# Performance work log

Measured on AMD Instinct MI355X. Metric: run time of the kernel, lower is better.

The kernel has to match this reference:

```python
import jax, jax.numpy as jnp
import numpy as np

MARGIN = 0.8  # TripletMarginMiner(margin=0.8, type_of_triplets='semihard')
Z_DIM = 512
N_CONCEPT = 64
NUM_TASK, NUM_SHOT, NUM_WAY = 16, 5, 5


def _triplet_indices(num_shot, num_way):
    # labels = torch.arange(num_way).repeat(num_shot) -> tile pattern
    labels = np.tile(np.arange(num_way), num_shot)
    N = labels.shape[0]
    same = labels[:, None] == labels[None, :]
    pos = same & ~np.eye(N, dtype=bool)          # a != p, same label
    neg = ~same                                  # different label
    a, p, n = np.nonzero(pos[:, :, None] & neg[:, None, :])  # all candidate triplets
    return jnp.asarray(a), jnp.asarray(p), jnp.asarray(n)


def setup_inputs() -> dict:
    key = jax.random.key(0)
    ks = jax.random.split(key, 12)
    d = Z_DIM
    s = lambda fan: 1.0 / np.sqrt(fan)
    inp = {
        'input_data': jax.random.normal(ks[0], (NUM_TASK, NUM_SHOT, NUM_WAY, d), jnp.float32),
        # proj_inner: Linear(3d -> 2d), ReLU, Linear(2d -> d)
        'W1': jax.random.normal(ks[1], (3 * d, 2 * d), jnp.float32) * s(3 * d),
        'b1': jnp.zeros((2 * d,), jnp.float32),
        'W2': jax.random.normal(ks[2], (2 * d, d), jnp.float32) * s(2 * d),
        'b2': jnp.zeros((d,), jnp.float32),
        # proj_outer: Linear(d -> 2d), ReLU, Linear(2d -> d)
        'W3': jax.random.normal(ks[3], (d, 2 * d), jnp.float32) * s(d),
        'b3': jnp.zeros((2 * d,), jnp.float32),
        'W4': jax.random.normal(ks[4], (2 * d, d), jnp.float32) * s(2 * d),
        'b4': jnp.zeros((d,), jnp.float32),
        # cls: Linear(d -> n_concept)
        'Wc': jax.random.normal(ks[5], (d, N_CONCEPT), jnp.float32) * s(d),
        'bc': jnp.zeros((N_CONCEPT,), jnp.float32),
    }
    return inp


def reference(input_data, W1, b1, W2, b2, W3, b3, W4, b4, Wc, bc):
    num_task, num_shot, num_way, d = input_data.shape
    x = input_data.reshape(num_task, num_shot * num_way, d)  # [K, N, d]
    a, p, n = _triplet_indices(num_shot, num_way)            # fixed triplet set [T]

    # --- semihard mining (no grad; binary mask so no grad path anyway) ---
    # LpDistance default: normalize embeddings, then L2 distance
    xn = x / jnp.linalg.norm(x, axis=-1, keepdims=True)
    sq = jnp.sum(xn * xn, axis=-1)                           # [K, N]
    D2 = sq[:, :, None] + sq[:, None, :] - 2.0 * jnp.einsum('kid,kjd->kij', xn, xn)
    D = jnp.sqrt(jnp.clip(D2, 0.0))                          # [K, N, N]
    tm = D[:, a, n] - D[:, a, p]                             # an_dist - ap_dist, [K, T]
    mask = ((tm > 0.0) & (tm <= MARGIN)).astype(x.dtype)     # semihard: 0 < margin <= 0.8

    # --- gather triplet embeddings (unnormalized), concat [x_a, x_p, x_n] ---
    feat = jnp.concatenate([x[:, a], x[:, p], x[:, n]], axis=-1)  # [K, T, 3d]

    # proj_inner then masked sum over mined triplets per task
    h = jax.nn.relu(feat @ W1 + b1) @ W2 + b2                # [K, T, d]
    pooled = jnp.einsum('ktd,kt->kd', h, mask)               # [K, d]

    o = jax.nn.relu(pooled @ W3 + b3) @ W4 + b4              # [K, d]
    score = o @ Wc + bc                                      # [K, n_concept]
    return jax.nn.softmax(score, axis=-1)
```

## Files before the change

### kernel.cpp

```cpp
#include <hip/hip_runtime.h>
#include <math.h>

#define NT 16
#define NR 25
#define DZ 512
#define D2Z 1024
#define NC 64

typedef short bf16x8 __attribute__((ext_vector_type(8)));
typedef float f32x4  __attribute__((ext_vector_type(4)));

#define TP  76
#define XSP 520
#define XP2 136
#define CP  68

static __device__ inline unsigned short f2bf(float v) {
    union { float f; unsigned u; } x; x.f = v;
    unsigned r = x.u + 0x7fffu + ((x.u >> 16) & 1u);
    return (unsigned short)(r >> 16);
}
static __device__ inline float bf2f(unsigned short h) {
    union { float f; unsigned u; } x; x.u = ((unsigned)h) << 16; return x.f;
}

__global__ __launch_bounds__(256) void k_prep(
    const float* __restrict__ x, const float* __restrict__ W1,
    unsigned short* __restrict__ W1h, unsigned short* __restrict__ W1l,
    float* __restrict__ Dm)
{
    __shared__ unsigned short th[64 * TP], tl[64 * TP];
    int vb = blockIdx.x;
    int tid = threadIdx.x;

    if (vb < 384) {
        int r0 = (vb % 24) * 64;
        int j0 = (vb / 24) * 64;
        int c  = r0 >> 9;
        int rb = r0 & 511;

        #pragma unroll
        for (int it = 0; it < 4; it++) {
            int rl = (tid >> 4) + it * 16;
            int jj = (tid & 15) * 4;
            float4 v = *(const float4*)(W1 + (size_t)(r0 + rl) * D2Z + j0 + jj);
            unsigned short h0 = f2bf(v.x), h1 = f2bf(v.y), h2 = f2bf(v.z), h3 = f2bf(v.w);
            th[rl * TP + jj + 0] = h0; tl[rl * TP + jj + 0] = f2bf(v.x - bf2f(h0));
            th[rl * TP + jj + 1] = h1; tl[rl * TP + jj + 1] = f2bf(v.y - bf2f(h1));
            th[rl * TP + jj + 2] = h2; tl[rl * TP + jj + 2] = f2bf(v.z - bf2f(h2));
            th[rl * TP + jj + 3] = h3; tl[rl * TP + jj + 3] = f2bf(v.w - bf2f(h3));
        }
        __syncthreads();

        #pragma unroll
        for (int it = 0; it < 4; it++) {
            int jl = (tid >> 4) + it * 16;
            int r4 = (tid & 15) * 4;
            ushort4 hv = make_ushort4(th[(r4+0)*TP + jl], th[(r4+1)*TP + jl],
                                      th[(r4+2)*TP + jl], th[(r4+3)*TP + jl]);
            ushort4 lv = make_ushort4(tl[(r4+0)*TP + jl], tl[(r4+1)*TP + jl],
                                      tl[(r4+2)*TP + jl], tl[(r4+3)*TP + jl]);
            size_t dst = ((size_t)c * D2Z + j0 + jl) * DZ + rb + r4;
            *(ushort4*)(W1h + dst) = hv;
            *(ushort4*)(W1l + dst) = lv;
        }
    } else {
        int i = vb - 384;
        int k = i & 15, a = i >> 4;
        int lane = tid & 63;
        int w    = tid >> 6;
        const float* xk = x + (size_t)k * NR * DZ;

        const float4* xap = (const float4*)(xk + a * DZ);
        float4 a0 = xap[lane];
        float4 a1 = xap[lane + 64];

        float sa = a0.x*a0.x + a0.y*a0.y + a0.z*a0.z + a0.w*a0.w
                 + a1.x*a1.x + a1.y*a1.y + a1.z*a1.z + a1.w*a1.w;
        #pragma unroll
        for (int off = 32; off; off >>= 1) sa += __shfl_xor(sa, off);
        float inva = 1.0f / sqrtf(sa);
        a0.x *= inva; a0.y *= inva; a0.z *= inva; a0.w *= inva;
        a1.x *= inva; a1.y *= inva; a1.z *= inva; a1.w *= inva;
        float sqa = a0.x*a0.x + a0.y*a0.y + a0.z*a0.z + a0.w*a0.w
                  + a1.x*a1.x + a1.y*a1.y + a1.z*a1.z + a1.w*a1.w;
        #pragma unroll
        for (int off = 32; off; off >>= 1) sqa += __shfl_xor(sqa, off);

        for (int j = w; j < NR; j += 4) {
            const float4* xjp = (const float4*)(xk + j * DZ);
            float4 j0 = xjp[lane];
            float4 j1 = xjp[lane + 64];
            float sj = j0.x*j0.x + j0.y*j0.y + j0.z*j0.z + j0.w*j0.w
                     + j1.x*j1.x + j1.y*j1.y + j1.z*j1.z + j1.w*j1.w;
            #pragma unroll
            for (int off = 32; off; off >>= 1) sj += __shfl_xor(sj, off);
            float invj = 1.0f / sqrtf(sj);
            j0.x *= invj; j0.y *= invj; j0.z *= invj; j0.w *= invj;
            j1.x *= invj; j1.y *= invj; j1.z *= invj; j1.w *= invj;

            float sqj = j0.x*j0.x + j0.y*j0.y + j0.z*j0.z + j0.w*j0.w
                      + j1.x*j1.x + j1.y*j1.y + j1.z*j1.z + j1.w*j1.w;
            float dij = a0.x*j0.x + a0.y*j0.y + a0.z*j0.z + a0.w*j0.w
                      + a1.x*j1.x + a1.y*j1.y + a1.z*j1.z + a1.w*j1.w;
            #pragma unroll
            for (int off = 32; off; off >>= 1) {
                sqj += __shfl_xor(sqj, off);
                dij += __shfl_xor(dij, off);
            }
            float d2 = sqa + sqj - 2.0f * dij;
            float d  = sqrtf(fmaxf(d2, 0.0f));
            if (lane == 0) Dm[((size_t)k * NR + a) * NR + j] = d;
        }
    }
}

__global__ __launch_bounds__(256) void k_fused(
    const float* __restrict__ x,
    const unsigned short* __restrict__ W1h, const unsigned short* __restrict__ W1l,
    const float* __restrict__ b1, const float* __restrict__ Dm,
    float* __restrict__ G)
{
    __shared__ unsigned short xs_h[26 * XSP], xs_l[26 * XSP];
    __shared__ unsigned short ws_h[64 * XP2], ws_l[64 * XP2];
    __shared__ float Ct[96 * CP];
    __shared__ float Dm_s[NR * NR];
    __shared__ float red[4][64];

    int bid = blockIdx.x;
    int k  = bid >> 4;
    int jt = bid & 15;
    int j0 = jt * 64;

    int tid  = threadIdx.x;
    int lane = tid & 63;
    int w    = tid >> 6;
    int q    = lane >> 4;
    int ln16 = lane & 15;

    for (int idx = tid; idx < NR * NR; idx += 256)
        Dm_s[idx] = Dm[(size_t)k * NR * NR + idx];

    for (int g = tid; g < NR * 64; g += 256) {
        int row = g >> 6;
        int c8  = (g & 63) * 8;
        const float* xp = x + ((size_t)k * NR + row) * DZ + c8;
        float4 v0 = *(const float4*)(xp);
        float4 v1 = *(const float4*)(xp + 4);
        unsigned short h;
        ushort4 ha, hb, la, lb;
        h = f2bf(v0.x); ha.x = h; la.x = f2bf(v0.x - bf2f(h));
        h = f2bf(v0.y); ha.y = h; la.y = f2bf(v0.y - bf2f(h));
        h = f2bf(v0.z); ha.z = h; la.z = f2bf(v0.z - bf2f(h));
        h = f2bf(v0.w); ha.w = h; la.w = f2bf(v0.w - bf2f(h));
        h = f2bf(v1.x); hb.x = h; lb.x = f2bf(v1.x - bf2f(h));
        h = f2bf(v1.y); hb.y = h; lb.y = f2bf(v1.y - bf2f(h));
        h = f2bf(v1.z); hb.z = h; lb.z = f2bf(v1.z - bf2f(h));
        h = f2bf(v1.w); hb.w = h; lb.w = f2bf(v1.w - bf2f(h));
        *(ushort4*)&xs_h[row * XSP + c8]     = ha;
        *(ushort4*)&xs_h[row * XSP + c8 + 4] = hb;
        *(ushort4*)&xs_l[row * XSP + c8]     = la;
        *(ushort4*)&xs_l[row * XSP + c8 + 4] = lb;
    }
    for (int g = tid; g < DZ; g += 256) {
        xs_h[25 * XSP + g] = 0;
        xs_l[25 * XSP + g] = 0;
    }

    int rowA1 = 16 + ln16;
    if (rowA1 > 25) rowA1 = 25;

    for (int c = 0; c < 3; c++) {
        f32x4 acc0 = (f32x4){0.f,0.f,0.f,0.f};
        f32x4 acc1 = (f32x4){0.f,0.f,0.f,0.f};

        for (int kk = 0; kk < 4; kk++) {
            int kbase = kk * 128;
            #pragma unroll
            for (int it = 0; it < 4; it++) {
                int g   = tid + 256 * it;
                int row = g >> 4;
                int kg  = (g & 15) * 8;
                size_t off = ((size_t)(c << 10) + j0 + row) * DZ + kbase + kg;
                *(uint4*)&ws_h[row * XP2 + kg] = *(const uint4*)(W1h + off);
                *(uint4*)&ws_l[row * XP2 + kg] = *(const uint4*)(W1l + off);
            }
            __syncthreads();

            #pragma unroll
            for (int ks = 0; ks < 4; ks++) {
                int ko  = ks * 32 + q * 8;
                int kog = kbase + ko;
                bf16x8 b_h = *(const bf16x8*)&ws_h[(w * 16 + ln16) * XP2 + ko];
                bf16x8 b_l = *(const bf16x8*)&ws_l[(w * 16 + ln16) * XP2 + ko];
                {
                    bf16x8 a_h = *(const bf16x8*)&xs_h[ln16 * XSP + kog];
                    bf16x8 a_l = *(const bf16x8*)&xs_l[ln16 * XSP + kog];
                    acc0 = __builtin_amdgcn_mfma_f32_16x16x32_bf16(a_h, b_h, acc0, 0, 0, 0);
                    acc0 = __builtin_amdgcn_mfma_f32_16x16x32_bf16(a_h, b_l, acc0, 0, 0, 0);
                    acc0 = __builtin_amdgcn_mfma_f32_16x16x32_bf16(a_l, b_h, acc0, 0, 0, 0);
                }
                {
                    bf16x8 a_h = *(const bf16x8*)&xs_h[rowA1 * XSP + kog];
                    bf16x8 a_l = *(const bf16x8*)&xs_l[rowA1 * XSP + kog];
                    acc1 = __builtin_amdgcn_mfma_f32_16x16x32_bf16(a_h, b_h, acc1, 0, 0, 0);
                    acc1 = __builtin_amdgcn_mfma_f32_16x16x32_bf16(a_h, b_l, acc1, 0, 0, 0);
                    acc1 = __builtin_amdgcn_mfma_f32_16x16x32_bf16(a_l, b_h, acc1, 0, 0, 0);
                }
            }
            __syncthreads();
        }

        int col = w * 16 + ln16;
        #pragma unroll
        for (int r = 0; r < 4; r++) {
            Ct[(c * 32 + q * 4 + r) * CP + col]      = acc0[r];
            Ct[(c * 32 + 16 + q * 4 + r) * CP + col] = acc1[r];
        }
    }
    __syncthreads();

    int j = tid & 63;
    int h = tid >> 6;
    float b1v = b1[j0 + j];

    float a2v[NR], a3v[NR];
    #pragma unroll
    for (int i = 0; i < NR; i++) a2v[i] = Ct[(32 + i) * CP + j];
    #pragma unroll
    for (int i = 0; i < NR; i++) a3v[i] = Ct[(64 + i) * CP + j];

    float acc = 0.0f;
    #pragma unroll
    for (int a = 0; a < NR; a++) {
        const int qa = a % 5, mdiv = a / 5;
        int m = h + (h >= mdiv);
        int p = qa + 5 * m;
        float a1  = Ct[a * CP + j];
        float dap = Dm_s[a * NR + p];
        float s = a1 + a2v[p] + b1v;
        #pragma unroll
        for (int ng = 0; ng < 5; ng++) {
            #pragma unroll
            for (int o = 0; o < 4; o++) {
                int n = ng * 5 + o + (o >= qa);
                float tm = Dm_s[a * NR + n] - dap;
                bool sel = (tm > 0.0f) && (tm <= 0.8f);
                float pre = fmaxf(s + a3v[n], 0.0f);
                float msk = sel ? 1.0f : 0.0f;
                acc = fmaf(msk, pre, acc);
            }
        }
    }
    red[h][j] = acc;
    __syncthreads();
    if (tid < 64)
        G[(size_t)k * D2Z + j0 + tid] = red[0][tid] + red[1][tid]
                                      + red[2][tid] + red[3][tid];
}

__global__ __launch_bounds__(256) void k_pooled(const float* __restrict__ G,
                                                const float* __restrict__ Dm,
                                                const float* __restrict__ W2,
                                                const float* __restrict__ b2,
                                                float* __restrict__ pooled)
{
    int bx = blockIdx.x, k = blockIdx.y;
    int tid = threadIdx.x, lane = tid & 63, kc = tid >> 6;
    int col = bx * 64 + lane;

    const float* Dk = Dm + (size_t)k * NR * NR;
    float cntv = 0.0f;
    for (int idx = tid; idx < 2000; idx += 256) {
        int a   = idx / 80;
        int rem = idx - a * 80;
        int mi  = rem / 20;
        int nn  = rem - mi * 20;
        int qa = a % 5, mdiv = a / 5;
        int m = mi + (mi >= mdiv);
        int p = qa + 5 * m;
        int ng = nn >> 2, o = nn & 3;
        int n = ng * 5 + o + (o >= qa);
        float tm = Dk[a * NR + n] - Dk[a * NR + p];
        cntv += ((tm > 0.0f) && (tm <= 0.8f)) ? 1.0f : 0.0f;
    }
    #pragma unroll
    for (int off = 32; off; off >>= 1) cntv += __shfl_xor(cntv, off);

    __shared__ float red[4][64];
    __shared__ float cred[4];
    if (lane == 0) cred[kc] = cntv;

    const float* Gk = G + (size_t)k * D2Z;
    float a0 = 0.f, a1 = 0.f, a2 = 0.f, a3 = 0.f;
    int j0 = kc * 256;
    #pragma unroll 4
    for (int jj = j0; jj < j0 + 256; jj += 4) {
        a0 = fmaf(Gk[jj+0], W2[(size_t)(jj+0) * DZ + col], a0);
        a1 = fmaf(Gk[jj+1], W2[(size_t)(jj+1) * DZ + col], a1);
        a2 = fmaf(Gk[jj+2], W2[(size_t)(jj+2) * DZ + col], a2);
        a3 = fmaf(Gk[jj+3], W2[(size_t)(jj+3) * DZ + col], a3);
    }
    red[kc][lane] = (a0 + a1) + (a2 + a3);
    __syncthreads();
    if (tid < 64) {
        float cnt = cred[0] + cred[1] + cred[2] + cred[3];
        float s = red[0][lane] + red[1][lane] + red[2][lane] + red[3][lane];
        s += cnt * b2[col];
        pooled[(size_t)k * DZ + col] = s;
    }
}

__global__ __launch_bounds__(256) void k_u(const float* __restrict__ pooled,
                                           const float* __restrict__ W3,
                                           const float* __restrict__ b3,
                                           float* __restrict__ u)
{
    int bx = blockIdx.x, k = blockIdx.y;
    int tid = threadIdx.x, lane = tid & 63, kc = tid >> 6;
    int col = bx * 64 + lane;

    const float* Pk = pooled + (size_t)k * DZ;
    float a0 = 0.f, a1 = 0.f, a2 = 0.f, a3 = 0.f;
    int s0 = kc * 128;
    #pragma unroll 4
    for (int s = s0; s < s0 + 128; s += 4) {
        a0 = fmaf(Pk[s+0], W3[(size_t)(s+0) * D2Z + col], a0);
        a1 = fmaf(Pk[s+1], W3[(size_t)(s+1) * D2Z + col], a1);
        a2 = fmaf(Pk[s+2], W3[(size_t)(s+2) * D2Z + col], a2);
        a3 = fmaf(Pk[s+3], W3[(size_t)(s+3) * D2Z + col], a3);
    }
    __shared__ float red[4][64];
    red[kc][lane] = (a0 + a1) + (a2 + a3);
    __syncthreads();
    if (tid < 64) {
        float v = red[0][lane] + red[1][lane] + red[2][lane] + red[3][lane] + b3[col];
        u[(size_t)k * D2Z + col] = fmaxf(v, 0.0f);
    }
}

__global__ __launch_bounds__(256) void k_o(const float* __restrict__ u,
                                           const float* __restrict__ W4,
                                           const float* __restrict__ b4,
                                           float* __restrict__ o)
{
    int bx = blockIdx.x, k = blockIdx.y;
    int tid = threadIdx.x, lane = tid & 63, kc = tid >> 6;
    int col = bx * 64 + lane;

    const float* Uk = u + (size_t)k * D2Z;
    float a0 = 0.f, a1 = 0.f, a2 = 0.f, a3 = 0.f;
    int j0 = kc * 256;
    #pragma unroll 4
    for (int jj = j0; jj < j0 + 256; jj += 4) {
        a0 = fmaf(Uk[jj+0], W4[(size_t)(jj+0) * DZ + col], a0);
        a1 = fmaf(Uk[jj+1], W4[(size_t)(jj+1) * DZ + col], a1);
        a2 = fmaf(Uk[jj+2], W4[(size_t)(jj+2) * DZ + col], a2);
        a3 = fmaf(Uk[jj+3], W4[(size_t)(jj+3) * DZ + col], a3);
    }
    __shared__ float red[4][64];
    red[kc][lane] = (a0 + a1) + (a2 + a3);
    __syncthreads();
    if (tid < 64) {
        o[(size_t)k * DZ + col] = red[0][lane] + red[1][lane] + red[2][lane]
                                + red[3][lane] + b4[col];
    }
}

__global__ __launch_bounds__(256) void k_score(const float* __restrict__ o,
                                               const float* __restrict__ Wc,
                                               const float* __restrict__ bc,
                                               float* __restrict__ out)
{
    int k = blockIdx.x;
    int tid = threadIdx.x, oc = tid & 63, kc = tid >> 6;

    const float* Ok = o + (size_t)k * DZ;
    float a0 = 0.f, a1 = 0.f, a2 = 0.f, a3 = 0.f;
    int r0 = kc * 128;
    #pragma unroll 4
    for (int rr = r0; rr < r0 + 128; rr += 4) {
        a0 = fmaf(Ok[rr+0], Wc[(size_t)(rr+0) * NC + oc], a0);
        a1 = fmaf(Ok[rr+1], Wc[(size_t)(rr+1) * NC + oc], a1);
        a2 = fmaf(Ok[rr+2], Wc[(size_t)(rr+2) * NC + oc], a2);
        a3 = fmaf(Ok[rr+3], Wc[(size_t)(rr+3) * NC + oc], a3);
    }
    __shared__ float red[4][64];
    red[kc][oc] = (a0 + a1) + (a2 + a3);
    __syncthreads();
    if (tid < 64) {
        float sc = bc[tid] + red[0][tid] + red[1][tid] + red[2][tid] + red[3][tid];
        float m = sc;
        #pragma unroll
        for (int off = 32; off; off >>= 1) m = fmaxf(m, __shfl_xor(m, off));
        float e = expf(sc - m);
        float ss = e;
        #pragma unroll
        for (int off = 32; off; off >>= 1) ss += __shfl_xor(ss, off);
        out[k * NC + tid] = e / ss;
    }
}

extern "C" void kernel_launch(void* const* d_in, const int* in_sizes, int n_in,
                              void* d_out, int out_size, void* d_ws, size_t ws_size,
                              hipStream_t stream)
{
    const float* x  = (const float*)d_in[0];
    const float* W1 = (const float*)d_in[1];
    const float* b1 = (const float*)d_in[2];
    const float* W2 = (const float*)d_in[3];
    const float* b2 = (const float*)d_in[4];
    const float* W3 = (const float*)d_in[5];
    const float* b3 = (const float*)d_in[6];
    const float* W4 = (const float*)d_in[7];
    const float* b4 = (const float*)d_in[8];
    const float* Wc = (const float*)d_in[9];
    const float* bc = (const float*)d_in[10];
    float* out = (float*)d_out;

    float* ws     = (float*)d_ws;
    float* Dm     = ws;
    float* G      = ws + 10016;
    float* pooled = ws + 26400;
    float* uu     = pooled + 8192;
    float* oo     = uu + 16384;
    unsigned short* W1h = (unsigned short*)(oo + 8192);
    unsigned short* W1l = W1h + 3 * D2Z * DZ;

    k_prep  <<<784,            256, 0, stream>>>(x, W1, W1h, W1l, Dm);
    k_fused <<<256,            256, 0, stream>>>(x, W1h, W1l, b1, Dm, G);
    k_pooled<<<dim3(8, NT),    256, 0, stream>>>(G, Dm, W2, b2, pooled);
    k_u     <<<dim3(16, NT),   256, 0, stream>>>(pooled, W3, b3, uu);
    k_o     <<<dim3(8, NT),    256, 0, stream>>>(uu, W4, b4, oo);
    k_score <<<NT,             256, 0, stream>>>(oo, Wc, bc, out);
}
```

Before: 151.5 us.

## Load W1 MFMA operands directly from global memory, drop LDS staging and syncs

```diff
diff --git a/kernel.cpp b/kernel.cpp
--- a/kernel.cpp
+++ b/kernel.cpp
@@ -12,7 +12,6 @@
 
 #define TP  76
 #define XSP 520
-#define XP2 136
 #define CP  68
 
 static __device__ inline unsigned short f2bf(float v) {
@@ -115,15 +114,14 @@
     }
 }
 
-__global__ __launch_bounds__(256) void k_fused(
+__global__ __launch_bounds__(256, 2) void k_fused(
     const float* __restrict__ x,
     const unsigned short* __restrict__ W1h, const unsigned short* __restrict__ W1l,
     const float* __restrict__ b1, const float* __restrict__ Dm,
     float* __restrict__ G)
 {
-    __shared__ unsigned short xs_h[26 * XSP], xs_l[26 * XSP];
-    __shared__ unsigned short ws_h[64 * XP2], ws_l[64 * XP2];
-    __shared__ float Ct[96 * CP];
+    __shared__ unsigned short xs_h[25 * XSP], xs_l[25 * XSP];
+    __shared__ float Ct[75 * CP];
     __shared__ float Dm_s[NR * NR];
     __shared__ float red[4][64];
 
@@ -162,60 +160,44 @@
         *(ushort4*)&xs_l[row * XSP + c8]     = la;
         *(ushort4*)&xs_l[row * XSP + c8 + 4] = lb;
     }
-    for (int g = tid; g < DZ; g += 256) {
-        xs_h[25 * XSP + g] = 0;
-        xs_l[25 * XSP + g] = 0;
-    }
+    __syncthreads();
 
     int rowA1 = 16 + ln16;
-    if (rowA1 > 25) rowA1 = 25;
+    if (rowA1 > 24) rowA1 = 24;
+
+    const unsigned short* wb_h = W1h + ((size_t)j0 + w * 16 + ln16) * DZ + q * 8;
+    const unsigned short* wb_l = W1l + ((size_t)j0 + w * 16 + ln16) * DZ + q * 8;
 
     for (int c = 0; c < 3; c++) {
         f32x4 acc0 = (f32x4){0.f,0.f,0.f,0.f};
         f32x4 acc1 = (f32x4){0.f,0.f,0.f,0.f};
-
-        for (int kk = 0; kk < 4; kk++) {
-            int kbase = kk * 128;
-            #pragma unroll
-            for (int it = 0; it < 4; it++) {
-                int g   = tid + 256 * it;
-                int row = g >> 4;
-                int kg  = (g & 15) * 8;
-                size_t off = ((size_t)(c << 10) + j0 + row) * DZ + kbase + kg;
-                *(uint4*)&ws_h[row * XP2 + kg] = *(const uint4*)(W1h + off);
-                *(uint4*)&ws_l[row * XP2 + kg] = *(const uint4*)(W1l + off);
-            }
-            __syncthreads();
-
-            #pragma unroll
-            for (int ks = 0; ks < 4; ks++) {
-                int ko  = ks * 32 + q * 8;
-                int kog = kbase + ko;
-                bf16x8 b_h = *(const bf16x8*)&ws_h[(w * 16 + ln16) * XP2 + ko];
-                bf16x8 b_l = *(const bf16x8*)&ws_l[(w * 16 + ln16) * XP2 + ko];
-                {
-                    bf16x8 a_h = *(const bf16x8*)&xs_h[ln16 * XSP + kog];
-                    bf16x8 a_l = *(const bf16x8*)&xs_l[ln16 * XSP + kog];
-                    acc0 = __builtin_amdgcn_mfma_f32_16x16x32_bf16(a_h, b_h, acc0, 0, 0, 0);
-                    acc0 = __builtin_amdgcn_mfma_f32_16x16x32_bf16(a_h, b_l, acc0, 0, 0, 0);
-                    acc0 = __builtin_amdgcn_mfma_f32_16x16x32_bf16(a_l, b_h, acc0, 0, 0, 0);
-                }
-                {
-                    bf16x8 a_h = *(const bf16x8*)&xs_h[rowA1 * XSP + kog];
-                    bf16x8 a_l = *(const bf16x8*)&xs_l[rowA1 * XSP + kog];
-                    acc1 = __builtin_amdgcn_mfma_f32_16x16x32_bf16(a_h, b_h, acc1, 0, 0, 0);
-                    acc1 = __builtin_amdgcn_mfma_f32_16x16x32_bf16(a_h, b_l, acc1, 0, 0, 0);
-                    acc1 = __builtin_amdgcn_mfma_f32_16x16x32_bf16(a_l, b_h, acc1, 0, 0, 0);
-                }
-            }
-            __syncthreads();
+        const unsigned short* wch = wb_h + (size_t)c * D2Z * DZ;
+        const unsigned short* wcl = wb_l + (size_t)c * D2Z * DZ;
+
+        #pragma unroll
+        for (int kc = 0; kc < 16; kc++) {
+            int kog = kc * 32 + q * 8;
+            bf16x8 b_h = *(const bf16x8*)(wch + kc * 32);
+            bf16x8 b_l = *(const bf16x8*)(wcl + kc * 32);
+            bf16x8 a0h = *(const bf16x8*)&xs_h[ln16 * XSP + kog];
+            bf16x8 a0l = *(const bf16x8*)&xs_l[ln16 * XSP + kog];
+            bf16x8 a1h = *(const bf16x8*)&xs_h[rowA1 * XSP + kog];
+            bf16x8 a1l = *(const bf16x8*)&xs_l[rowA1 * XSP + kog];
+            acc0 = __builtin_amdgcn_mfma_f32_16x16x32_bf16(a0h, b_h, acc0, 0, 0, 0);
+            acc0 = __builtin_amdgcn_mfma_f32_16x16x32_bf16(a0h, b_l, acc0, 0, 0, 0);
+            acc0 = __builtin_amdgcn_mfma_f32_16x16x32_bf16(a0l, b_h, acc0, 0, 0, 0);
+            acc1 = __builtin_amdgcn_mfma_f32_16x16x32_bf16(a1h, b_h, acc1, 0, 0, 0);
+            acc1 = __builtin_amdgcn_mfma_f32_16x16x32_bf16(a1h, b_l, acc1, 0, 0, 0);
+            acc1 = __builtin_amdgcn_mfma_f32_16x16x32_bf16(a1l, b_h, acc1, 0, 0, 0);
         }
 
         int col = w * 16 + ln16;
         #pragma unroll
         for (int r = 0; r < 4; r++) {
-            Ct[(c * 32 + q * 4 + r) * CP + col]      = acc0[r];
-            Ct[(c * 32 + 16 + q * 4 + r) * CP + col] = acc1[r];
+            int r0 = q * 4 + r;
+            Ct[(c * 25 + r0) * CP + col] = acc0[r];
+            int r1 = 16 + q * 4 + r;
+            if (r1 < 25) Ct[(c * 25 + r1) * CP + col] = acc1[r];
         }
     }
     __syncthreads();
@@ -226,9 +208,9 @@
 
     float a2v[NR], a3v[NR];
     #pragma unroll
-    for (int i = 0; i < NR; i++) a2v[i] = Ct[(32 + i) * CP + j];
+    for (int i = 0; i < NR; i++) a2v[i] = Ct[(25 + i) * CP + j];
     #pragma unroll
-    for (int i = 0; i < NR; i++) a3v[i] = Ct[(64 + i) * CP + j];
+    for (int i = 0; i < NR; i++) a3v[i] = Ct[(50 + i) * CP + j];
 
     float acc = 0.0f;
     #pragma unroll
```

Result: no change. 151.7 us, median of 2 (+0.1%).
